# Optimization experiments

Hardware: AMD Instinct MI355X
Metric: run time of the kernel (lower is better)

Reference implementation:

```python
import jax, jax.numpy as jnp
import numpy as np

HALF = 1          # half_size
KS = 2 * HALF + 1 # kernel size = 3
ALPHA = 0.05
ITER = 10
LOG_N = float(np.log(KS * KS))
EPS = 1e-8


def _dilate(x):
    # x: [B, 1, H, W] -- soft (log-sum-exp-like) dilation with entropy correction.
    B, C, H, W = x.shape
    xp = jnp.pad(x, ((0, 0), (0, 0), (HALF, HALF), (HALF, HALF)), mode='reflect')
    # Extract ks*ks shifted views -> patches [B, K, H, W] (C == 1 folded away);
    # ordering (ki, kj) matches torch.nn.Unfold's channel-major layout for C=1.
    patches = jnp.stack(
        [xp[:, 0, i:i + H, j:j + W] for i in range(KS) for j in range(KS)],
        axis=1,
    )
    w = jax.nn.softmax(patches / ALPHA, axis=1)
    weighted_sum = jnp.sum(patches * w, axis=1)                 # [B, H, W]
    entropy = -jnp.sum(w * jnp.log(w + EPS), axis=1)            # [B, H, W]
    out = weighted_sum + ALPHA * (entropy - LOG_N)
    return out[:, None, :, :]                                   # [B, 1, H, W]


def _erode(x):
    return -_dilate(-x)


def _open(x):
    return _dilate(_erode(x))


def _forward(x):
    skel = jnp.clip(x - _open(x), 0.0, 1.0)

    def step(carry, _):
        xc, sk = carry
        xc = _erode(xc)
        sk = sk + jnp.clip(xc - _open(xc), 0.0, 1.0)
        return (xc, sk), None

    (_, skel), _ = jax.lax.scan(step, (x, skel), None, length=ITER)
    return skel


def setup_inputs() -> dict:
    key = jax.random.key(0)
    x = jax.random.uniform(key, (2, 1, 1024, 1024), dtype=jnp.float32)
    return {"x": x}


def reference(x):
    return _forward(x)
```

## Files before the change

kernel.cpp:

```cpp
#include <hip/hip_runtime.h>


#define HH 1024
#define WW 1024
#define NB 2
#define OTX 104
#define OTY 88
#define TW 128
#define TH 112
#define RPW 7
#define NW 16
#define HALO 12
#define GX 10
#define GY 12

constexpr float C1 = 28.85390081777927f;
constexpr float C2 = 0.03465735902799726f;

typedef float f32x2 __attribute__((ext_vector_type(2)));

__device__ __forceinline__ int mir(int i, int n) {
    return i < 0 ? -i : (i >= n ? 2 * n - 2 - i : i);
}
__device__ __forceinline__ float nbrL(float v) {
    return __int_as_float(__builtin_amdgcn_update_dpp(
        0, __float_as_int(v), 0x138, 0xf, 0xf, true));
}
__device__ __forceinline__ float nbrR(float v) {
    return __int_as_float(__builtin_amdgcn_update_dpp(
        0, __float_as_int(v), 0x130, 0xf, 0xf, true));
}

__device__ __forceinline__ f32x2 pk_add(f32x2 a, f32x2 b) {
    f32x2 d;
    asm("v_pk_add_f32 %0, %1, %2" : "=v"(d) : "v"(a), "v"(b));
    return d;
}
__device__ __forceinline__ f32x2 pk_add_swapB(f32x2 a, f32x2 b) {
    f32x2 d;
    asm("v_pk_add_f32 %0, %1, %2 op_sel:[0,1] op_sel_hi:[1,0]"
        : "=v"(d) : "v"(a), "v"(b));
    return d;
}
__device__ __forceinline__ f32x2 pk_mul(f32x2 a, f32x2 b) {
    f32x2 d;
    asm("v_pk_mul_f32 %0, %1, %2" : "=v"(d) : "v"(a), "v"(b));
    return d;
}

__device__ __forceinline__ f32x2 hsum3p(f32x2 P) {
    f32x2 LR;
    LR.x = nbrL(P.y);
    LR.y = nbrR(P.x);
    f32x2 X = pk_add(LR, P);
    return pk_add_swapB(X, P);
}

__global__ __launch_bounds__(1024, 4) void skel_k(const float* __restrict__ x0,
                                                  float* __restrict__ out) {
    __shared__ f32x2 halo[2][NW][4][64];
    const int lane = threadIdx.x & 63;
    const int w    = threadIdx.x >> 6;
    const int tx = blockIdx.x, ty = blockIdx.y, b = blockIdx.z;
    const int gx0 = tx * OTX - HALO, gy0 = ty * OTY - HALO;
    const int r0 = w * RPW;

    const float* src = x0 + (size_t)b * HH * WW;

    f32x2 a0, a1, a2, a3, a4, a5, a6;
    const bool interior = (gx0 >= 0) && (gx0 + TW <= WW) &&
                          (gy0 >= 0) && (gy0 + TH <= HH);
    if (interior) {
        const float* base = src + (size_t)(gy0 + r0) * WW + gx0 + 2 * lane;
#define LOADROW(I, AV) { f32x2 v_ = *reinterpret_cast<const f32x2*>(base + (size_t)(I) * WW); \
        AV.x = __builtin_amdgcn_exp2f(v_.x * -C1); \
        AV.y = __builtin_amdgcn_exp2f(v_.y * -C1); }
        LOADROW(0, a0) LOADROW(1, a1) LOADROW(2, a2) LOADROW(3, a3)
        LOADROW(4, a4) LOADROW(5, a5) LOADROW(6, a6)
#undef LOADROW
    } else {
        const int mx0 = mir(gx0 + 2 * lane, WW);
        const int mx1 = mir(gx0 + 2 * lane + 1, WW);
#define LOADROW(I, AV) { int my_ = mir(gy0 + r0 + (I), HH); \
        const float* rr_ = src + (size_t)my_ * WW; \
        AV.x = __builtin_amdgcn_exp2f(rr_[mx0] * -C1); \
        AV.y = __builtin_amdgcn_exp2f(rr_[mx1] * -C1); }
        LOADROW(0, a0) LOADROW(1, a1) LOADROW(2, a2) LOADROW(3, a3)
        LOADROW(4, a4) LOADROW(5, a5) LOADROW(6, a6)
#undef LOADROW
    }

    f32x2 s0 = {0.f, 0.f}, s1 = s0, s2 = s0, s3 = s0, s4 = s0,
          s5 = s0, s6 = s0;

    const bool hasTerm = (r0 + RPW - 1 >= HALO) && (r0 < TH - HALO);
#define OKT(I) ((r0 + (I) >= HALO) && (r0 + (I) < TH - HALO))
    const bool ok0 = OKT(0), ok1 = OKT(1), ok2 = OKT(2), ok3 = OKT(3),
               ok4 = OKT(4), ok5 = OKT(5), ok6 = OKT(6);
#undef OKT

    #pragma unroll 1
    for (int j = 0; j < 11; ++j) {
        const int p = j & 1;
        halo[p][w][0][lane] = a0;
        halo[p][w][1][lane] = a1;
        halo[p][w][2][lane] = a5;
        halo[p][w][3][lane] = a6;
        __syncthreads();
        f32x2 one2 = {1.f, 1.f};
        f32x2 hm2 = (w > 0)      ? halo[p][w - 1][2][lane] : one2;
        f32x2 hm1 = (w > 0)      ? halo[p][w - 1][3][lane] : one2;
        f32x2 hp0 = (w < NW - 1) ? halo[p][w + 1][0][lane] : one2;
        f32x2 hp1 = (w < NW - 1) ? halo[p][w + 1][1][lane] : one2;

        f32x2 h_m = hsum3p(hm2);
        f32x2 h_c = hsum3p(hm1);
        f32x2 n_prev = {0.f, 0.f};

        if (hasTerm) {
            f32x2 r_2 = {0.f, 0.f}, r_1 = r_2;
#define STEPC(OP1) \
            f32x2 h_p = hsum3p(OP1); \
            f32x2 n   = pk_add(pk_add(h_m, h_c), h_p); \
            f32x2 rc; rc.x = __builtin_amdgcn_rcpf(n.x); \
                      rc.y = __builtin_amdgcn_rcpf(n.y); \
            f32x2 r_0 = hsum3p(rc);
#define STEP0(OP1) { STEPC(OP1) \
            n_prev = n; h_m = h_c; h_c = h_p; r_2 = r_1; r_1 = r_0; }
#define STEP(OP1, AT, ST, OKb) { STEPC(OP1) \
            if (OKb) { \
                f32x2 rs = pk_add(pk_add(r_2, r_1), r_0); \
                f32x2 PS = pk_mul(AT, rs); \
                f32x2 t; \
                t.x = __builtin_amdgcn_fmed3f(-C2 * __builtin_amdgcn_logf(PS.x), 0.f, 1.f); \
                t.y = __builtin_amdgcn_fmed3f(-C2 * __builtin_amdgcn_logf(PS.y), 0.f, 1.f); \
                ST = pk_add(ST, t); \
            } \
            AT = n_prev; \
            n_prev = n; h_m = h_c; h_c = h_p; r_2 = r_1; r_1 = r_0; }

            STEP0(a0)
            STEP0(a1)
            STEP(a2,  a0, s0, ok0)
            STEP(a3,  a1, s1, ok1)
            STEP(a4,  a2, s2, ok2)
            STEP(a5,  a3, s3, ok3)
            STEP(a6,  a4, s4, ok4)
            STEP(hp0, a5, s5, ok5)
            STEP(hp1, a6, s6, ok6)
#undef STEP
#undef STEP0
#undef STEPC
        } else {
#define BSTEP0(OP1) { f32x2 h_p = hsum3p(OP1); \
            f32x2 n = pk_add(pk_add(h_m, h_c), h_p); \
            n_prev = n; h_m = h_c; h_c = h_p; }
#define BSTEP(OP1, AT) { f32x2 h_p = hsum3p(OP1); \
            f32x2 n = pk_add(pk_add(h_m, h_c), h_p); \
            AT = n_prev; n_prev = n; h_m = h_c; h_c = h_p; }
            BSTEP0(a0)
            BSTEP0(a1)
            BSTEP(a2,  a0)
            BSTEP(a3,  a1)
            BSTEP(a4,  a2)
            BSTEP(a5,  a3)
            BSTEP(a6,  a4)
            BSTEP(hp0, a5)
            BSTEP(hp1, a6)
#undef BSTEP
#undef BSTEP0
        }
    }

    if (hasTerm && lane >= 6 && lane <= 57) {
        int gx = gx0 + 2 * lane;
        if (gx >= 0 && gx + 1 < WW) {
            float* dst = out + (size_t)b * HH * WW;
#define STOREROW(I, SV) { int trow = r0 + (I); \
            if (trow >= HALO && trow < TH - HALO) { \
                int gy = gy0 + trow; \
                if (gy < HH) \
                    *reinterpret_cast<f32x2*>(&dst[(size_t)gy * WW + gx]) = SV; } }
            STOREROW(0, s0) STOREROW(1, s1) STOREROW(2, s2) STOREROW(3, s3)
            STOREROW(4, s4) STOREROW(5, s5) STOREROW(6, s6)
#undef STOREROW
        }
    }
}

extern "C" void kernel_launch(void* const* d_in, const int* in_sizes, int n_in,
                              void* d_out, int out_size, void* d_ws, size_t ws_size,
                              hipStream_t stream) {
    const float* x0 = (const float*)d_in[0];
    float* skel = (float*)d_out;
    skel_k<<<dim3(GX, GY, NB), dim3(1024, 1, 1), 0, stream>>>(x0, skel);
}
```

Measured before the change: 28.68 us.

## Rebalance rows across waves so halo rows sit in dedicated box-only waves

The uniform 7-rows-per-wave split is replaced by an uneven one. Waves 0 and 15 each hold 12 halo rows and only run the cheap box-sum path. Four waves take 7 output rows and ten take 6, so the rcp/log skeleton work is spread evenly over 14 waves and the per-row output predicates go away. The inline-asm packed add and mul helpers are swapped for plain vector arithmetic, and hsum3p is rewritten to share one partial sum. The cost is higher register pressure from 12 row registers in the box waves and more divergent code paths by wave role.

```diff
diff --git a/kernel.cpp b/kernel.cpp
--- a/kernel.cpp
+++ b/kernel.cpp
@@ -8,7 +8,6 @@
 #define OTY 88
 #define TW 128
 #define TH 112
-#define RPW 7
 #define NW 16
 #define HALO 12
 #define GX 10
@@ -31,29 +30,12 @@
         0, __float_as_int(v), 0x130, 0xf, 0xf, true));
 }
 
-__device__ __forceinline__ f32x2 pk_add(f32x2 a, f32x2 b) {
-    f32x2 d;
-    asm("v_pk_add_f32 %0, %1, %2" : "=v"(d) : "v"(a), "v"(b));
-    return d;
-}
-__device__ __forceinline__ f32x2 pk_add_swapB(f32x2 a, f32x2 b) {
-    f32x2 d;
-    asm("v_pk_add_f32 %0, %1, %2 op_sel:[0,1] op_sel_hi:[1,0]"
-        : "=v"(d) : "v"(a), "v"(b));
-    return d;
-}
-__device__ __forceinline__ f32x2 pk_mul(f32x2 a, f32x2 b) {
-    f32x2 d;
-    asm("v_pk_mul_f32 %0, %1, %2" : "=v"(d) : "v"(a), "v"(b));
-    return d;
-}
-
 __device__ __forceinline__ f32x2 hsum3p(f32x2 P) {
+    float s = P.x + P.y;
     f32x2 LR;
-    LR.x = nbrL(P.y);
-    LR.y = nbrR(P.x);
-    f32x2 X = pk_add(LR, P);
-    return pk_add_swapB(X, P);
+    LR.x = nbrL(P.y) + s;
+    LR.y = nbrR(P.x) + s;
+    return LR;
 }
 
 __global__ __launch_bounds__(1024, 4) void skel_k(const float* __restrict__ x0,
@@ -63,49 +45,49 @@
     const int w    = threadIdx.x >> 6;
     const int tx = blockIdx.x, ty = blockIdx.y, b = blockIdx.z;
     const int gx0 = tx * OTX - HALO, gy0 = ty * OTY - HALO;
-    const int r0 = w * RPW;
+    const int r0 = (w == 0) ? 0
+                 : (w <= 4) ? 12 + 7 * (w - 1)
+                 : (w <= 14) ? 40 + 6 * (w - 5) : 100;
+    const bool isBox = (w == 0) || (w == 15);
+    const bool is7   = (w >= 1) && (w <= 4);
 
     const float* src = x0 + (size_t)b * HH * WW;
-
-    f32x2 a0, a1, a2, a3, a4, a5, a6;
     const bool interior = (gx0 >= 0) && (gx0 + TW <= WW) &&
                           (gy0 >= 0) && (gy0 + TH <= HH);
-    if (interior) {
-        const float* base = src + (size_t)(gy0 + r0) * WW + gx0 + 2 * lane;
-#define LOADROW(I, AV) { f32x2 v_ = *reinterpret_cast<const f32x2*>(base + (size_t)(I) * WW); \
+    const int mx0 = mir(gx0 + 2 * lane, WW);
+    const int mx1 = mir(gx0 + 2 * lane + 1, WW);
+    const float* base = src + (size_t)(gy0 + r0) * WW + gx0 + 2 * lane;
+
+    f32x2 a0, a1, a2, a3, a4, a5, a6, a7, a8, a9, a10, a11;
+#define LD(I, AV) { \
+    if (interior) { \
+        f32x2 v_ = *reinterpret_cast<const f32x2*>(base + (size_t)(I) * WW); \
         AV.x = __builtin_amdgcn_exp2f(v_.x * -C1); \
-        AV.y = __builtin_amdgcn_exp2f(v_.y * -C1); }
-        LOADROW(0, a0) LOADROW(1, a1) LOADROW(2, a2) LOADROW(3, a3)
-        LOADROW(4, a4) LOADROW(5, a5) LOADROW(6, a6)
-#undef LOADROW
-    } else {
-        const int mx0 = mir(gx0 + 2 * lane, WW);
-        const int mx1 = mir(gx0 + 2 * lane + 1, WW);
-#define LOADROW(I, AV) { int my_ = mir(gy0 + r0 + (I), HH); \
+        AV.y = __builtin_amdgcn_exp2f(v_.y * -C1); \
+    } else { \
+        int my_ = mir(gy0 + r0 + (I), HH); \
         const float* rr_ = src + (size_t)my_ * WW; \
         AV.x = __builtin_amdgcn_exp2f(rr_[mx0] * -C1); \
-        AV.y = __builtin_amdgcn_exp2f(rr_[mx1] * -C1); }
-        LOADROW(0, a0) LOADROW(1, a1) LOADROW(2, a2) LOADROW(3, a3)
-        LOADROW(4, a4) LOADROW(5, a5) LOADROW(6, a6)
-#undef LOADROW
-    }
+        AV.y = __builtin_amdgcn_exp2f(rr_[mx1] * -C1); \
+    } }
+    LD(0, a0) LD(1, a1) LD(2, a2) LD(3, a3) LD(4, a4) LD(5, a5)
+    if (isBox) { LD(6, a6) LD(7, a7) LD(8, a8) LD(9, a9) LD(10, a10) LD(11, a11) }
+    else if (is7) { LD(6, a6) }
+#undef LD
 
-    f32x2 s0 = {0.f, 0.f}, s1 = s0, s2 = s0, s3 = s0, s4 = s0,
-          s5 = s0, s6 = s0;
-
-    const bool hasTerm = (r0 + RPW - 1 >= HALO) && (r0 < TH - HALO);
-#define OKT(I) ((r0 + (I) >= HALO) && (r0 + (I) < TH - HALO))
-    const bool ok0 = OKT(0), ok1 = OKT(1), ok2 = OKT(2), ok3 = OKT(3),
-               ok4 = OKT(4), ok5 = OKT(5), ok6 = OKT(6);
-#undef OKT
+    f32x2 s0 = {0.f, 0.f}, s1 = s0, s2 = s0, s3 = s0, s4 = s0, s5 = s0, s6 = s0;
 
     #pragma unroll 1
     for (int j = 0; j < 11; ++j) {
         const int p = j & 1;
+        f32x2 pub2, pub3;
+        if (isBox)    { pub2 = a10; pub3 = a11; }
+        else if (is7) { pub2 = a5;  pub3 = a6;  }
+        else          { pub2 = a4;  pub3 = a5;  }
         halo[p][w][0][lane] = a0;
         halo[p][w][1][lane] = a1;
-        halo[p][w][2][lane] = a5;
-        halo[p][w][3][lane] = a6;
+        halo[p][w][2][lane] = pub2;
+        halo[p][w][3][lane] = pub3;
         __syncthreads();
         f32x2 one2 = {1.f, 1.f};
         f32x2 hm2 = (w > 0)      ? halo[p][w - 1][2][lane] : one2;
@@ -117,46 +99,48 @@
         f32x2 h_c = hsum3p(hm1);
         f32x2 n_prev = {0.f, 0.f};
 
-        if (hasTerm) {
+        if (!isBox) {
             f32x2 r_2 = {0.f, 0.f}, r_1 = r_2;
 #define STEPC(OP1) \
             f32x2 h_p = hsum3p(OP1); \
-            f32x2 n   = pk_add(pk_add(h_m, h_c), h_p); \
+            f32x2 n   = h_m + h_c + h_p; \
             f32x2 rc; rc.x = __builtin_amdgcn_rcpf(n.x); \
                       rc.y = __builtin_amdgcn_rcpf(n.y); \
             f32x2 r_0 = hsum3p(rc);
 #define STEP0(OP1) { STEPC(OP1) \
             n_prev = n; h_m = h_c; h_c = h_p; r_2 = r_1; r_1 = r_0; }
-#define STEP(OP1, AT, ST, OKb) { STEPC(OP1) \
-            if (OKb) { \
-                f32x2 rs = pk_add(pk_add(r_2, r_1), r_0); \
-                f32x2 PS = pk_mul(AT, rs); \
-                f32x2 t; \
-                t.x = __builtin_amdgcn_fmed3f(-C2 * __builtin_amdgcn_logf(PS.x), 0.f, 1.f); \
-                t.y = __builtin_amdgcn_fmed3f(-C2 * __builtin_amdgcn_logf(PS.y), 0.f, 1.f); \
-                ST = pk_add(ST, t); \
-            } \
+#define STEP(OP1, AT, ST) { STEPC(OP1) \
+            f32x2 PS = AT * (r_2 + r_1 + r_0); \
+            f32x2 t; \
+            t.x = __builtin_amdgcn_fmed3f(-C2 * __builtin_amdgcn_logf(PS.x), 0.f, 1.f); \
+            t.y = __builtin_amdgcn_fmed3f(-C2 * __builtin_amdgcn_logf(PS.y), 0.f, 1.f); \
+            ST += t; \
             AT = n_prev; \
             n_prev = n; h_m = h_c; h_c = h_p; r_2 = r_1; r_1 = r_0; }
 
             STEP0(a0)
             STEP0(a1)
-            STEP(a2,  a0, s0, ok0)
-            STEP(a3,  a1, s1, ok1)
-            STEP(a4,  a2, s2, ok2)
-            STEP(a5,  a3, s3, ok3)
-            STEP(a6,  a4, s4, ok4)
-            STEP(hp0, a5, s5, ok5)
-            STEP(hp1, a6, s6, ok6)
+            STEP(a2, a0, s0)
+            STEP(a3, a1, s1)
+            STEP(a4, a2, s2)
+            STEP(a5, a3, s3)
+            if (is7) {
+                STEP(a6,  a4, s4)
+                STEP(hp0, a5, s5)
+                STEP(hp1, a6, s6)
+            } else {
+                STEP(hp0, a4, s4)
+                STEP(hp1, a5, s5)
+            }
 #undef STEP
 #undef STEP0
 #undef STEPC
         } else {
 #define BSTEP0(OP1) { f32x2 h_p = hsum3p(OP1); \
-            f32x2 n = pk_add(pk_add(h_m, h_c), h_p); \
+            f32x2 n = h_m + h_c + h_p; \
             n_prev = n; h_m = h_c; h_c = h_p; }
 #define BSTEP(OP1, AT) { f32x2 h_p = hsum3p(OP1); \
-            f32x2 n = pk_add(pk_add(h_m, h_c), h_p); \
+            f32x2 n = h_m + h_c + h_p; \
             AT = n_prev; n_prev = n; h_m = h_c; h_c = h_p; }
             BSTEP0(a0)
             BSTEP0(a1)
@@ -165,25 +149,29 @@
             BSTEP(a4,  a2)
             BSTEP(a5,  a3)
             BSTEP(a6,  a4)
-            BSTEP(hp0, a5)
-            BSTEP(hp1, a6)
+            BSTEP(a7,  a5)
+            BSTEP(a8,  a6)
+            BSTEP(a9,  a7)
+            BSTEP(a10, a8)
+            BSTEP(a11, a9)
+            BSTEP(hp0, a10)
+            BSTEP(hp1, a11)
 #undef BSTEP
 #undef BSTEP0
         }
     }
 
-    if (hasTerm && lane >= 6 && lane <= 57) {
+    if (!isBox && lane >= 6 && lane <= 57) {
         int gx = gx0 + 2 * lane;
-        if (gx >= 0 && gx + 1 < WW) {
+        if (gx + 1 < WW) {
             float* dst = out + (size_t)b * HH * WW;
-#define STOREROW(I, SV) { int trow = r0 + (I); \
-            if (trow >= HALO && trow < TH - HALO) { \
-                int gy = gy0 + trow; \
-                if (gy < HH) \
-                    *reinterpret_cast<f32x2*>(&dst[(size_t)gy * WW + gx]) = SV; } }
-            STOREROW(0, s0) STOREROW(1, s1) STOREROW(2, s2) STOREROW(3, s3)
-            STOREROW(4, s4) STOREROW(5, s5) STOREROW(6, s6)
-#undef STOREROW
+#define STORE(I, SV) { int gy = gy0 + r0 + (I); \
+            if (gy < HH) \
+                *reinterpret_cast<f32x2*>(&dst[(size_t)gy * WW + gx]) = SV; }
+            STORE(0, s0) STORE(1, s1) STORE(2, s2) STORE(3, s3)
+            STORE(4, s4) STORE(5, s5)
+            if (is7) { STORE(6, s6) }
+#undef STORE
         }
     }
 }
```

New measurement: 29.14 us. No clear change (+1.6%).
